# Kernel optimization log

Measured on AMD Instinct MI355X. Metric: run time of the kernel, lower is better.

## Reference

```python
import jax, jax.numpy as jnp
import numpy as np

# dims
B, T = 256, 64
N_AG, N_FEAT = 10, 4
X_DIM, X_PERM, X_STATIC = 44, 40, 10
HID, XEMB, NHID = 128, 32, 8
E = N_AG * (N_AG - 1)           # 90 directed edges (off-diagonal)
GEMB = NHID * E                 # 720 graph embedding per sample/step
RNN_IN = XEMB + 1 + GEMB        # 753
A_IN = X_STATIC + GEMB          # 730 (x_emb_size2==0 in GraphNN branch)
O_IN = XEMB + X_STATIC + 1 + GEMB  # 763

_off = np.ones((N_AG, N_AG)) - np.eye(N_AG)
RECV = jnp.asarray(np.where(_off)[0])  # rel_rec one-hot == gather by receiver idx
SEND = jnp.asarray(np.where(_off)[1])  # rel_send one-hot == gather by sender idx


def setup_inputs() -> dict:
    key = jax.random.key(0)
    ks = jax.random.split(key, 32)
    w = lambda k, shape: jax.random.normal(k, shape, jnp.float32) * 0.05
    return {
        'x': jax.random.normal(ks[0], (B, T + 1, X_DIM), jnp.float32),
        'x_demo': jax.random.normal(ks[1], (B, X_STATIC), jnp.float32),
        'f_treatment': jax.random.uniform(ks[2], (B, T + 1, 1), jnp.float32),
        'h0': jax.random.normal(ks[3], (B, HID), jnp.float32),
        # x2emb (Linear 4->32), x_static2emb (Linear 10->10)
        'W_x2emb': w(ks[4], (XEMB, X_DIM - X_PERM)), 'b_x2emb': w(ks[5], (XEMB,)),
        'W_stat': w(ks[6], (X_STATIC, X_STATIC)), 'b_stat': w(ks[7], (X_STATIC,)),
        # NRI-style MLP1 (node): 4->8->8 ; MLP2 (edge): 16->8->8
        'W_m1a': w(ks[8], (NHID, N_FEAT)), 'b_m1a': w(ks[9], (NHID,)),
        'W_m1b': w(ks[10], (NHID, NHID)), 'b_m1b': w(ks[11], (NHID,)),
        'W_m2a': w(ks[12], (NHID, 2 * NHID)), 'b_m2a': w(ks[13], (NHID,)),
        'W_m2b': w(ks[14], (NHID, NHID)), 'b_m2b': w(ks[15], (NHID,)),
        # treatment head: Linear(730->128)+ReLU, then Linear(128->1, no bias)
        'W_a1': w(ks[16], (HID, A_IN)), 'b_a1': w(ks[17], (HID,)),
        'W_a2': w(ks[18], (1, HID)),
        # outcome head: Linear(763->128)+ReLU, then Linear(128->1, no bias)
        'W_o1': w(ks[19], (HID, O_IN)), 'b_o1': w(ks[20], (HID,)),
        'W_o2': w(ks[21], (1, HID)),
        # GRUCell(753 -> 128)
        'W_ih': w(ks[22], (3 * HID, RNN_IN)), 'b_ih': w(ks[23], (3 * HID,)),
        'W_hh': w(ks[24], (3 * HID, HID)), 'b_hh': w(ks[25], (3 * HID,)),
    }


def reference(x, x_demo, f_treatment, h0, W_x2emb, b_x2emb, W_stat, b_stat,
              W_m1a, b_m1a, W_m1b, b_m1b, W_m2a, b_m2a, W_m2b, b_m2b,
              W_a1, b_a1, W_a2, W_o1, b_o1, W_o2, W_ih, b_ih, W_hh, b_hh):
    xt = x[:, :T]                       # (B,T,44); len_time = x.size(1)-1
    treat = f_treatment[:, :T]          # (B,T,1)
    demo = x_demo @ W_stat.T + b_stat   # (B,10) static embedding
    demoT = jnp.broadcast_to(demo[:, None], (B, T, X_STATIC))

    # --- GNN(x_permuted): mlp1 per node, node2edge gather, mlp2 per edge ---
    xa = xt[..., :X_PERM].reshape(B, T, N_AG, N_FEAT)
    h1 = jax.nn.elu(xa @ W_m1a.T + b_m1a)
    h1 = jax.nn.elu(h1 @ W_m1b.T + b_m1b)         # (B,T,N_AG,8); BN in eval = identity
    edges = jnp.concatenate([h1[:, :, RECV], h1[:, :, SEND]], axis=-1)  # (B,T,E,16)
    h2 = jax.nn.elu(edges @ W_m2a.T + b_m2a)
    h2 = jax.nn.elu(h2 @ W_m2b.T + b_m2b)         # (B,T,E,8)
    gemb = h2.reshape(B, T, GEMB)                 # (B,T,720)

    xemb = xt[..., X_PERM:] @ W_x2emb.T + b_x2emb  # (B,T,32)

    # --- treatment (a_or_ipw) head; dropout identity in eval ---
    a_in = jnp.concatenate([demoT, gemb], axis=-1)          # (B,T,730)
    a_out = jax.nn.relu(a_in @ W_a1.T + b_a1) @ W_a2.T      # (B,T,1)

    # --- outcome head ---
    o_in = jnp.concatenate([xemb, demoT, treat, gemb], axis=-1)  # (B,T,763)
    y_out = jax.nn.relu(o_in @ W_o1.T + b_o1) @ W_o2.T           # (B,T,1)

    # --- GRUCell recurrence over time ---
    rnn_in = jnp.concatenate([xemb, treat, gemb], axis=-1)  # (B,T,753)
    gi = rnn_in @ W_ih.T + b_ih                             # precompute input proj (B,T,3H)

    def step(h, g):
        gh = h @ W_hh.T + b_hh
        i_r, i_z, i_n = jnp.split(g, 3, axis=-1)
        h_r, h_z, h_n = jnp.split(gh, 3, axis=-1)
        r = jax.nn.sigmoid(i_r + h_r)
        z = jax.nn.sigmoid(i_z + h_z)
        n = jnp.tanh(i_n + r * h_n)
        h_new = (1.0 - z) * n + z * h
        return h_new, h_new

    _, hs = jax.lax.scan(step, h0, jnp.swapaxes(gi, 0, 1))
    hs = jnp.swapaxes(hs, 0, 1)                             # (B,T,128)

    return jnp.concatenate([a_out, y_out, hs], axis=-1)     # (B,T,130)
```

## Files before the change

### kernel.cpp

```cpp
#include <hip/hip_runtime.h>
#include <hip/hip_bf16.h>
#include <math.h>

#define BB     256
#define TT     64
#define BT     (BB*TT)
#define XD     44
#define XP     40
#define XS     10
#define HID    128
#define XEMB   32
#define NHID   8
#define NAG    10
#define NEDGE  90
#define GEMB   720
#define KF     768
#define NTOT   640

typedef __bf16  bf16_t;
typedef __bf16  bf16x8 __attribute__((ext_vector_type(8)));
typedef float   floatx4 __attribute__((ext_vector_type(4)));

__device__ __forceinline__ float elu_f(float v) { return v > 0.f ? v : expm1f(v); }
__device__ __forceinline__ float sigmoid_f(float v) { return 1.f / (1.f + expf(-v)); }

__global__ __launch_bounds__(256) void prep_kernel(
    const float* __restrict__ Wa1, const float* __restrict__ ba1,
    const float* __restrict__ Wo1, const float* __restrict__ bo1,
    const float* __restrict__ Wih, const float* __restrict__ bih,
    bf16_t* __restrict__ WT, float* __restrict__ bcat) {
  int idx = blockIdx.x * 256 + threadIdx.x;
  if (idx >= NTOT * KF) return;
  int n = idx / KF, k = idx - n * KF;
  float v = 0.f;
  if (n < 128) {
    if (k >= 32 && k < 42)        v = Wa1[n * 730 + (k - 32)];
    else if (k >= 43 && k < 763)  v = Wa1[n * 730 + 10 + (k - 43)];
  } else if (n < 256) {
    int m = n - 128;
    if (k < 763)                  v = Wo1[m * 763 + k];
  } else {
    int m = n - 256;
    if (k < 32)                   v = Wih[m * 753 + k];
    else if (k == 42)             v = Wih[m * 753 + 32];
    else if (k >= 43 && k < 763)  v = Wih[m * 753 + 33 + (k - 43)];
  }
  WT[n * KF + k] = (bf16_t)v;
  if (k == 0) {
    bcat[n] = (n < 128) ? ba1[n] : (n < 256 ? bo1[n - 128] : bih[n - 256]);
  }
}

#define W_M1A 0
#define B_M1A 32
#define W_M1B 40
#define B_M1B 104
#define W_M2A 112
#define B_M2A 240
#define W_M2B 248
#define B_M2B 312
#define W_X2E 320
#define B_X2E 448
#define W_ST  480
#define B_ST  580
#define W_TOT 590

__global__ __launch_bounds__(64) void encoder_kernel(
    const float* __restrict__ x, const float* __restrict__ x_demo,
    const float* __restrict__ ftreat,
    const float* __restrict__ Wm1a, const float* __restrict__ bm1a,
    const float* __restrict__ Wm1b, const float* __restrict__ bm1b,
    const float* __restrict__ Wm2a, const float* __restrict__ bm2a,
    const float* __restrict__ Wm2b, const float* __restrict__ bm2b,
    const float* __restrict__ Wx2e, const float* __restrict__ bx2e,
    const float* __restrict__ Wst, const float* __restrict__ bst,
    bf16_t* __restrict__ F) {
  int tok = blockIdx.x;
  int b = tok >> 6, t = tok & 63;
  int tid = threadIdx.x;

  __shared__ float w[W_TOT];
  __shared__ float xl[XD];
  __shared__ float h1a[NAG * 8];
  __shared__ float h1s[NAG * 8];
  __shared__ float h2a[NEDGE * 8];

  for (int i = tid; i < 32;  i += 64) w[W_M1A + i] = Wm1a[i];
  for (int i = tid; i < 8;   i += 64) w[B_M1A + i] = bm1a[i];
  for (int i = tid; i < 64;  i += 64) w[W_M1B + i] = Wm1b[i];
  for (int i = tid; i < 8;   i += 64) w[B_M1B + i] = bm1b[i];
  for (int i = tid; i < 128; i += 64) w[W_M2A + i] = Wm2a[i];
  for (int i = tid; i < 8;   i += 64) w[B_M2A + i] = bm2a[i];
  for (int i = tid; i < 64;  i += 64) w[W_M2B + i] = Wm2b[i];
  for (int i = tid; i < 8;   i += 64) w[B_M2B + i] = bm2b[i];
  for (int i = tid; i < 128; i += 64) w[W_X2E + i] = Wx2e[i];
  for (int i = tid; i < 32;  i += 64) w[B_X2E + i] = bx2e[i];
  for (int i = tid; i < 100; i += 64) w[W_ST + i]  = Wst[i];
  for (int i = tid; i < 10;  i += 64) w[B_ST + i]  = bst[i];
  if (tid < XD) xl[tid] = x[(size_t)(b * 65 + t) * XD + tid];
  __syncthreads();

  for (int c = tid; c < NAG * 8; c += 64) {
    int i = c >> 3, o = c & 7;
    float s = w[B_M1A + o];
#pragma unroll
    for (int f = 0; f < 4; f++) s += xl[i * 4 + f] * w[W_M1A + o * 4 + f];
    h1a[c] = elu_f(s);
  }
  __syncthreads();
  for (int c = tid; c < NAG * 8; c += 64) {
    int i = c >> 3, o = c & 7;
    float s = w[B_M1B + o];
#pragma unroll
    for (int p = 0; p < 8; p++) s += h1a[i * 8 + p] * w[W_M1B + o * 8 + p];
    h1s[c] = elu_f(s);
  }
  __syncthreads();
  for (int c = tid; c < NEDGE * 8; c += 64) {
    int e = c >> 3, o = c & 7;
    int r = e / 9, q = e - 9 * r;
    int sd = q + (q >= r ? 1 : 0);
    float s = w[B_M2A + o];
#pragma unroll
    for (int kk = 0; kk < 8; kk++) s += h1s[r * 8 + kk]  * w[W_M2A + o * 16 + kk];
#pragma unroll
    for (int kk = 0; kk < 8; kk++) s += h1s[sd * 8 + kk] * w[W_M2A + o * 16 + 8 + kk];
    h2a[c] = elu_f(s);
  }
  __syncthreads();

  bf16_t* Frow = F + (size_t)tok * KF;
  for (int c = tid; c < NEDGE * 8; c += 64) {
    int e = c >> 3, o = c & 7;
    float s = w[B_M2B + o];
#pragma unroll
    for (int kk = 0; kk < 8; kk++) s += h2a[e * 8 + kk] * w[W_M2B + o * 8 + kk];
    Frow[43 + c] = (bf16_t)elu_f(s);
  }
  if (tid < 32) {
    float s = w[B_X2E + tid];
#pragma unroll
    for (int f = 0; f < 4; f++) s += xl[40 + f] * w[W_X2E + tid * 4 + f];
    Frow[tid] = (bf16_t)s;
  } else if (tid < 42) {
    int d = tid - 32;
    float s = w[B_ST + d];
#pragma unroll
    for (int j = 0; j < 10; j++) s += x_demo[b * XS + j] * w[W_ST + d * 10 + j];
    Frow[tid] = (bf16_t)s;
  } else if (tid == 42) {
    Frow[42] = (bf16_t)ftreat[b * 65 + t];
  } else if (tid < 48) {
    Frow[720 + tid] = (bf16_t)0.f;
  }
}

__global__ __launch_bounds__(256) void gemm_kernel(
    const bf16_t* __restrict__ F, const bf16_t* __restrict__ WT,
    const float* __restrict__ bcat, float* __restrict__ G) {
  __shared__ __align__(16) bf16_t As[128 * 32];
  __shared__ __align__(16) bf16_t Bs[128 * 32];

  int tid  = threadIdx.x;
  int lane = tid & 63;
  int wv   = tid >> 6;
  int wr   = wv >> 1, wc = wv & 1;
  int m0 = blockIdx.x * 128, n0 = blockIdx.y * 128;

  floatx4 acc[4][4];
#pragma unroll
  for (int i = 0; i < 4; i++)
#pragma unroll
    for (int j = 0; j < 4; j++) acc[i][j] = floatx4{0.f, 0.f, 0.f, 0.f};

  int c0 = tid, c1 = tid + 256;
  int r0 = c0 >> 2, p0 = c0 & 3;
  int r1 = c1 >> 2, p1 = c1 & 3;
  int qr = lane >> 4;
  int lr = lane & 15;

  for (int k0 = 0; k0 < KF; k0 += 32) {
    uint4 a0 = *(const uint4*)(F  + (size_t)(m0 + r0) * KF + k0 + p0 * 8);
    uint4 a1 = *(const uint4*)(F  + (size_t)(m0 + r1) * KF + k0 + p1 * 8);
    uint4 b0 = *(const uint4*)(WT + (size_t)(n0 + r0) * KF + k0 + p0 * 8);
    uint4 b1 = *(const uint4*)(WT + (size_t)(n0 + r1) * KF + k0 + p1 * 8);
    __syncthreads();
    ((uint4*)As)[c0] = a0; ((uint4*)As)[c1] = a1;
    ((uint4*)Bs)[c0] = b0; ((uint4*)Bs)[c1] = b1;
    __syncthreads();

    bf16x8 af[4], bf[4];
#pragma unroll
    for (int i = 0; i < 4; i++) {
      af[i] = *(const bf16x8*)(As + (wr * 64 + i * 16 + lr) * 32 + qr * 8);
      bf[i] = *(const bf16x8*)(Bs + (wc * 64 + i * 16 + lr) * 32 + qr * 8);
    }
#pragma unroll
    for (int i = 0; i < 4; i++)
#pragma unroll
      for (int j = 0; j < 4; j++)
        acc[i][j] = __builtin_amdgcn_mfma_f32_16x16x32_bf16(af[i], bf[j], acc[i][j], 0, 0, 0);
  }

#pragma unroll
  for (int i = 0; i < 4; i++) {
#pragma unroll
    for (int j = 0; j < 4; j++) {
      int col = n0 + wc * 64 + j * 16 + lr;
      float bv = bcat[col];
#pragma unroll
      for (int r = 0; r < 4; r++) {
        int row = m0 + wr * 64 + i * 16 + qr * 4 + r;
        G[(size_t)row * NTOT + col] = acc[i][j][r] + bv;
      }
    }
  }
}

__global__ __launch_bounds__(256) void head_kernel(
    const float* __restrict__ G, const float* __restrict__ Wa2,
    const float* __restrict__ Wo2, float* __restrict__ out) {
  int wid  = (blockIdx.x * 256 + threadIdx.x) >> 6;
  int lane = threadIdx.x & 63;
  const float* g = G + (size_t)wid * NTOT;
  float sa = fmaxf(g[lane], 0.f) * Wa2[lane] + fmaxf(g[lane + 64], 0.f) * Wa2[lane + 64];
  float sy = fmaxf(g[128 + lane], 0.f) * Wo2[lane] + fmaxf(g[192 + lane], 0.f) * Wo2[lane + 64];
#pragma unroll
  for (int off = 32; off > 0; off >>= 1) {
    sa += __shfl_down(sa, off, 64);
    sy += __shfl_down(sy, off, 64);
  }
  if (lane == 0) {
    out[(size_t)wid * 130 + 0] = sa;
    out[(size_t)wid * 130 + 1] = sy;
  }
}

__global__ __launch_bounds__(384, 1) void gru_kernel(
    const float* __restrict__ G, const float* __restrict__ h0,
    const float* __restrict__ Whh, const float* __restrict__ bhh,
    float* __restrict__ out) {
  int b = blockIdx.x;
  int tid = threadIdx.x;

  __shared__ float hbuf[2][HID];
  __shared__ float gh[384];

  float wrow[HID];
#pragma unroll
  for (int k = 0; k < HID; k += 4) {
    float4 v = *(const float4*)(Whh + (size_t)tid * HID + k);
    wrow[k] = v.x; wrow[k + 1] = v.y; wrow[k + 2] = v.z; wrow[k + 3] = v.w;
  }
  float bias = bhh[tid];
  if (tid < HID) hbuf[0][tid] = h0[(size_t)b * HID + tid];
  __syncthreads();

  int cur = 0;
  for (int t = 0; t < TT; t++) {
    float s = 0.f;
#pragma unroll
    for (int k = 0; k < HID; k += 4) {
      float4 h4 = *(const float4*)(&hbuf[cur][k]);
      s += wrow[k] * h4.x + wrow[k + 1] * h4.y + wrow[k + 2] * h4.z + wrow[k + 3] * h4.w;
    }
    gh[tid] = s + bias;
    __syncthreads();
    if (tid < HID) {
      const float* grow = G + (size_t)(b * TT + t) * NTOT;
      float ir = grow[256 + tid], iz = grow[384 + tid], inn = grow[512 + tid];
      float r = sigmoid_f(ir + gh[tid]);
      float z = sigmoid_f(iz + gh[128 + tid]);
      float n = tanhf(inn + r * gh[256 + tid]);
      float hn = (1.f - z) * n + z * hbuf[cur][tid];
      hbuf[cur ^ 1][tid] = hn;
      out[(size_t)(b * TT + t) * 130 + 2 + tid] = hn;
    }
    __syncthreads();
    cur ^= 1;
  }
}

extern "C" void kernel_launch(void* const* d_in, const int* in_sizes, int n_in,
                              void* d_out, int out_size, void* d_ws, size_t ws_size,
                              hipStream_t stream) {
  const float* x      = (const float*)d_in[0];
  const float* x_demo = (const float*)d_in[1];
  const float* ftr    = (const float*)d_in[2];
  const float* h0     = (const float*)d_in[3];
  const float* Wx2e   = (const float*)d_in[4];
  const float* bx2e   = (const float*)d_in[5];
  const float* Wst    = (const float*)d_in[6];
  const float* bst    = (const float*)d_in[7];
  const float* Wm1a   = (const float*)d_in[8];
  const float* bm1a   = (const float*)d_in[9];
  const float* Wm1b   = (const float*)d_in[10];
  const float* bm1b   = (const float*)d_in[11];
  const float* Wm2a   = (const float*)d_in[12];
  const float* bm2a   = (const float*)d_in[13];
  const float* Wm2b   = (const float*)d_in[14];
  const float* bm2b   = (const float*)d_in[15];
  const float* Wa1    = (const float*)d_in[16];
  const float* ba1    = (const float*)d_in[17];
  const float* Wa2    = (const float*)d_in[18];
  const float* Wo1    = (const float*)d_in[19];
  const float* bo1    = (const float*)d_in[20];
  const float* Wo2    = (const float*)d_in[21];
  const float* Wih    = (const float*)d_in[22];
  const float* bih    = (const float*)d_in[23];
  const float* Whh    = (const float*)d_in[24];
  const float* bhh    = (const float*)d_in[25];
  float* out = (float*)d_out;

  char* ws = (char*)d_ws;
  bf16_t* F   = (bf16_t*)(ws);
  bf16_t* WT  = (bf16_t*)(ws + 25165824);
  float*  bc  = (float*)(ws + 25165824 + 983040);
  float*  G   = (float*)(ws + 25165824 + 983040 + 2560);

  prep_kernel<<<dim3((NTOT * KF + 255) / 256), dim3(256), 0, stream>>>(
      Wa1, ba1, Wo1, bo1, Wih, bih, WT, bc);
  encoder_kernel<<<dim3(BT), dim3(64), 0, stream>>>(
      x, x_demo, ftr, Wm1a, bm1a, Wm1b, bm1b, Wm2a, bm2a, Wm2b, bm2b,
      Wx2e, bx2e, Wst, bst, F);
  gemm_kernel<<<dim3(BT / 128, NTOT / 128), dim3(256), 0, stream>>>(F, WT, bc, G);
  head_kernel<<<dim3(BT / 4), dim3(256), 0, stream>>>(G, Wa2, Wo2, out);
  gru_kernel<<<dim3(BB), dim3(384), 0, stream>>>(G, h0, Whh, bhh, out);
}
```

Baseline: 280.1 us.

## Specialize GRU warps into matvec and gate groups with prefetched inputs

The GRU kernel grows to 512 threads. 384 threads compute the recurrent matvec, now split across four partial accumulators, while a separate group of 128 threads prefetches the next step's input-gate values from G and evaluates the gates. Sigmoid and tanh switch to fast exp/rcp approximations, and launch bounds change to (512,2). The aim is to hide global-load latency and shorten the serial per-step critical path, at some cost in tanh/sigmoid accuracy and in register pressure under the new bounds.

```diff
diff --git a/kernel.cpp b/kernel.cpp
--- a/kernel.cpp
+++ b/kernel.cpp
@@ -22,7 +22,9 @@
 typedef float   floatx4 __attribute__((ext_vector_type(4)));
 
 __device__ __forceinline__ float elu_f(float v) { return v > 0.f ? v : expm1f(v); }
-__device__ __forceinline__ float sigmoid_f(float v) { return 1.f / (1.f + expf(-v)); }
+__device__ __forceinline__ float rcp_fast(float x) { return __builtin_amdgcn_rcpf(x); }
+__device__ __forceinline__ float sigmoid_fast(float v) { return rcp_fast(1.f + __expf(-v)); }
+__device__ __forceinline__ float tanh_fast(float x) { return 1.f - 2.f * rcp_fast(1.f + __expf(2.f * x)); }
 
 __global__ __launch_bounds__(256) void prep_kernel(
     const float* __restrict__ Wa1, const float* __restrict__ ba1,
@@ -236,7 +238,7 @@
   }
 }
 
-__global__ __launch_bounds__(384, 1) void gru_kernel(
+__global__ __launch_bounds__(512, 2) void gru_kernel(
     const float* __restrict__ G, const float* __restrict__ h0,
     const float* __restrict__ Whh, const float* __restrict__ bhh,
     float* __restrict__ out) {
@@ -246,35 +248,60 @@
   __shared__ float hbuf[2][HID];
   __shared__ float gh[384];
 
+  bool is_mat = tid < 384;
+  int j = tid - 384;
+  const float* gbase = G + (size_t)b * TT * NTOT;
+
   float wrow[HID];
-#pragma unroll
-  for (int k = 0; k < HID; k += 4) {
-    float4 v = *(const float4*)(Whh + (size_t)tid * HID + k);
-    wrow[k] = v.x; wrow[k + 1] = v.y; wrow[k + 2] = v.z; wrow[k + 3] = v.w;
-  }
-  float bias = bhh[tid];
+  float bias = 0.f;
+  float ir = 0.f, iz = 0.f, inn = 0.f;
+  if (is_mat) {
+#pragma unroll
+    for (int k = 0; k < HID; k += 4) {
+      float4 v = *(const float4*)(Whh + (size_t)tid * HID + k);
+      wrow[k] = v.x; wrow[k + 1] = v.y; wrow[k + 2] = v.z; wrow[k + 3] = v.w;
+    }
+    bias = bhh[tid];
+  } else {
+    ir  = gbase[256 + j];
+    iz  = gbase[384 + j];
+    inn = gbase[512 + j];
+  }
   if (tid < HID) hbuf[0][tid] = h0[(size_t)b * HID + tid];
   __syncthreads();
 
   int cur = 0;
   for (int t = 0; t < TT; t++) {
-    float s = 0.f;
-#pragma unroll
-    for (int k = 0; k < HID; k += 4) {
-      float4 h4 = *(const float4*)(&hbuf[cur][k]);
-      s += wrow[k] * h4.x + wrow[k + 1] * h4.y + wrow[k + 2] * h4.z + wrow[k + 3] * h4.w;
-    }
-    gh[tid] = s + bias;
+    float nir = 0.f, niz = 0.f, ninn = 0.f;
+    if (is_mat) {
+      float s0 = 0.f, s1 = 0.f, s2 = 0.f, s3 = 0.f;
+#pragma unroll
+      for (int k = 0; k < HID; k += 16) {
+        float4 a = *(const float4*)(&hbuf[cur][k]);
+        float4 c = *(const float4*)(&hbuf[cur][k + 4]);
+        float4 d = *(const float4*)(&hbuf[cur][k + 8]);
+        float4 e = *(const float4*)(&hbuf[cur][k + 12]);
+        s0 += wrow[k] * a.x + wrow[k + 1] * a.y + wrow[k + 2] * a.z + wrow[k + 3] * a.w;
+        s1 += wrow[k + 4] * c.x + wrow[k + 5] * c.y + wrow[k + 6] * c.z + wrow[k + 7] * c.w;
+        s2 += wrow[k + 8] * d.x + wrow[k + 9] * d.y + wrow[k + 10] * d.z + wrow[k + 11] * d.w;
+        s3 += wrow[k + 12] * e.x + wrow[k + 13] * e.y + wrow[k + 14] * e.z + wrow[k + 15] * e.w;
+      }
+      gh[tid] = (s0 + s1) + (s2 + s3) + bias;
+    } else if (t + 1 < TT) {
+      const float* gn = gbase + (size_t)(t + 1) * NTOT;
+      nir  = gn[256 + j];
+      niz  = gn[384 + j];
+      ninn = gn[512 + j];
+    }
     __syncthreads();
-    if (tid < HID) {
-      const float* grow = G + (size_t)(b * TT + t) * NTOT;
-      float ir = grow[256 + tid], iz = grow[384 + tid], inn = grow[512 + tid];
-      float r = sigmoid_f(ir + gh[tid]);
-      float z = sigmoid_f(iz + gh[128 + tid]);
-      float n = tanhf(inn + r * gh[256 + tid]);
-      float hn = (1.f - z) * n + z * hbuf[cur][tid];
-      hbuf[cur ^ 1][tid] = hn;
-      out[(size_t)(b * TT + t) * 130 + 2 + tid] = hn;
+    if (!is_mat) {
+      float r  = sigmoid_fast(ir + gh[j]);
+      float z  = sigmoid_fast(iz + gh[128 + j]);
+      float nn = tanh_fast(inn + r * gh[256 + j]);
+      float hn = (1.f - z) * nn + z * hbuf[cur][j];
+      hbuf[cur ^ 1][j] = hn;
+      out[(size_t)(b * TT + t) * 130 + 2 + j] = hn;
+      ir = nir; iz = niz; inn = ninn;
     }
     __syncthreads();
     cur ^= 1;
@@ -325,5 +352,5 @@
       Wx2e, bx2e, Wst, bst, F);
   gemm_kernel<<<dim3(BT / 128, NTOT / 128), dim3(256), 0, stream>>>(F, WT, bc, G);
   head_kernel<<<dim3(BT / 4), dim3(256), 0, stream>>>(G, Wa2, Wo2, out);
-  gru_kernel<<<dim3(BB), dim3(384), 0, stream>>>(G, h0, Whh, bhh, out);
-}
+  gru_kernel<<<dim3(BB), dim3(512), 0, stream>>>(G, h0, Whh, bhh, out);
+}
```

Result: faster. 263.6 us (-5.9%).

## Use fp16 packed dot products, readlane broadcast, fast gates and prefetch in GRU

Applied to the files above, without the earlier changes.

The GRU recurrence kernel now keeps its recurrent weights as packed fp16 pairs and computes the hidden projection with fdot2 instructions. The hidden state is broadcast from a packed fp16 LDS array through readlane instead of float4 LDS loads. It also prefetches the next step's input-gate values, keeps the previous hidden value in a register, and replaces sigmoid and tanh with fast exp/rcp approximations. The aim is to shorten the serial per-step latency, at the cost of reduced precision in the weights, hidden state and activations.

```diff
diff --git a/kernel.cpp b/kernel.cpp
--- a/kernel.cpp
+++ b/kernel.cpp
@@ -20,9 +20,12 @@
 typedef __bf16  bf16_t;
 typedef __bf16  bf16x8 __attribute__((ext_vector_type(8)));
 typedef float   floatx4 __attribute__((ext_vector_type(4)));
+typedef _Float16 half2_t __attribute__((ext_vector_type(2)));
 
 __device__ __forceinline__ float elu_f(float v) { return v > 0.f ? v : expm1f(v); }
-__device__ __forceinline__ float sigmoid_f(float v) { return 1.f / (1.f + expf(-v)); }
+__device__ __forceinline__ float rcp_fast(float x) { return __builtin_amdgcn_rcpf(x); }
+__device__ __forceinline__ float sigmoid_fast(float v) { return rcp_fast(1.f + __expf(-v)); }
+__device__ __forceinline__ float tanh_fast(float x) { return 1.f - 2.f * rcp_fast(1.f + __expf(2.f * x)); }
 
 __global__ __launch_bounds__(256) void prep_kernel(
     const float* __restrict__ Wa1, const float* __restrict__ ba1,
@@ -242,42 +245,63 @@
     float* __restrict__ out) {
   int b = blockIdx.x;
   int tid = threadIdx.x;
-
-  __shared__ float hbuf[2][HID];
+  int lane = tid & 63;
+  bool gate = tid < HID;
+
   __shared__ float gh[384];
-
-  float wrow[HID];
+  __shared__ unsigned int h2[HID / 2];
+
+  const float* gbase = G + (size_t)b * TT * NTOT;
+
+  half2_t w2[64];
 #pragma unroll
   for (int k = 0; k < HID; k += 4) {
     float4 v = *(const float4*)(Whh + (size_t)tid * HID + k);
-    wrow[k] = v.x; wrow[k + 1] = v.y; wrow[k + 2] = v.z; wrow[k + 3] = v.w;
+    w2[k / 2]     = half2_t{(_Float16)v.x, (_Float16)v.y};
+    w2[k / 2 + 1] = half2_t{(_Float16)v.z, (_Float16)v.w};
   }
   float bias = bhh[tid];
-  if (tid < HID) hbuf[0][tid] = h0[(size_t)b * HID + tid];
-  __syncthreads();
-
-  int cur = 0;
+
+  float hprev = 0.f, ir = 0.f, iz = 0.f, inn = 0.f;
+  if (gate) {
+    hprev = h0[(size_t)b * HID + tid];
+    ((_Float16*)h2)[tid] = (_Float16)hprev;
+    ir  = gbase[256 + tid];
+    iz  = gbase[384 + tid];
+    inn = gbase[512 + tid];
+  }
+  __syncthreads();
+
   for (int t = 0; t < TT; t++) {
-    float s = 0.f;
-#pragma unroll
-    for (int k = 0; k < HID; k += 4) {
-      float4 h4 = *(const float4*)(&hbuf[cur][k]);
-      s += wrow[k] * h4.x + wrow[k + 1] * h4.y + wrow[k + 2] * h4.z + wrow[k + 3] * h4.w;
-    }
-    gh[tid] = s + bias;
+    unsigned int hl = h2[lane];
+    float nir = 0.f, niz = 0.f, ninn = 0.f;
+    if (gate && t + 1 < TT) {
+      const float* gn = gbase + (size_t)(t + 1) * NTOT;
+      nir  = gn[256 + tid];
+      niz  = gn[384 + tid];
+      ninn = gn[512 + tid];
+    }
+    float s0 = 0.f, s1 = 0.f;
+#pragma unroll
+    for (int k = 0; k < 64; k += 2) {
+      int p0 = __builtin_amdgcn_readlane((int)hl, k);
+      int p1 = __builtin_amdgcn_readlane((int)hl, k + 1);
+      s0 = __builtin_amdgcn_fdot2(w2[k],     __builtin_bit_cast(half2_t, p0), s0, false);
+      s1 = __builtin_amdgcn_fdot2(w2[k + 1], __builtin_bit_cast(half2_t, p1), s1, false);
+    }
+    gh[tid] = s0 + s1 + bias;
     __syncthreads();
-    if (tid < HID) {
-      const float* grow = G + (size_t)(b * TT + t) * NTOT;
-      float ir = grow[256 + tid], iz = grow[384 + tid], inn = grow[512 + tid];
-      float r = sigmoid_f(ir + gh[tid]);
-      float z = sigmoid_f(iz + gh[128 + tid]);
-      float n = tanhf(inn + r * gh[256 + tid]);
-      float hn = (1.f - z) * n + z * hbuf[cur][tid];
-      hbuf[cur ^ 1][tid] = hn;
+    if (gate) {
+      float r  = sigmoid_fast(ir + gh[tid]);
+      float z  = sigmoid_fast(iz + gh[HID + tid]);
+      float nn = tanh_fast(inn + r * gh[2 * HID + tid]);
+      float hn = (1.f - z) * nn + z * hprev;
+      hprev = hn;
       out[(size_t)(b * TT + t) * 130 + 2 + tid] = hn;
+      ((_Float16*)h2)[tid] = (_Float16)hn;
+      ir = nir; iz = niz; inn = ninn;
     }
     __syncthreads();
-    cur ^= 1;
   }
 }
 
```

After: 242.7 us. 1.15x faster.
